# Kernel tuning notes

Measured on AMD Instinct MI355X. Metric: run time of the kernel, lower is better.

The kernel has to match this reference:

```python
import jax, jax.numpy as jnp
import numpy as np

# Module / shape constants (match init_kwargs and forward-path constants)
H = 8          # heads
DH = 80        # dim_head
QDIM = 640     # query_dim == inner_dim (context = x, self-attention content branch)
B = 1
NQ = 2048      # query tokens
NS = 2048      # injected style tokens
T = 1.2        # injection_config['T']  (attn_matrix_scale)
GAMMA = 0.3    # injection_config['gamma'] (q_mix)
LAMBDA_MAX = 2.5
TOPK = 128     # style_topk
STYLE_SCALE = 1.0
SCALE = DH ** -0.5


def _split_heads(t, h):
    # 'b n (h d) -> (b h) n d'
    b, n, hd = t.shape
    return t.reshape(b, n, h, hd // h).transpose(0, 2, 1, 3).reshape(b * h, n, hd // h)


def setup_inputs() -> dict:
    key = jax.random.key(0)
    ks = jax.random.split(key, 9)
    x = jax.random.normal(ks[0], (B, NQ, QDIM), jnp.float32)
    Q_c_injected = jax.random.normal(ks[1], (H, NQ, DH), jnp.float32) * 0.5
    K_s_injected = jax.random.normal(ks[2], (H, NS, DH), jnp.float32) * 0.5
    V_s_injected = jax.random.normal(ks[3], (H, NS, DH), jnp.float32) * 0.5
    # Learned params (nn.Linear weights are [out, in]; no bias on q/k/v)
    Wq = jax.random.normal(ks[4], (H * DH, QDIM), jnp.float32) * 0.02
    Wk = jax.random.normal(ks[5], (H * DH, QDIM), jnp.float32) * 0.02
    Wv = jax.random.normal(ks[6], (H * DH, QDIM), jnp.float32) * 0.02
    Wo = jax.random.normal(ks[7], (QDIM, H * DH), jnp.float32) * 0.02
    bo = jnp.zeros((QDIM,), jnp.float32)
    ada_gate = jnp.array([0.2], jnp.float32)
    return {"x": x, "Q_c_injected": Q_c_injected, "K_s_injected": K_s_injected,
            "V_s_injected": V_s_injected, "Wq": Wq, "Wk": Wk, "Wv": Wv,
            "Wo": Wo, "bo": bo, "ada_gate": ada_gate}


def reference(x, Q_c_injected, K_s_injected, V_s_injected, Wq, Wk, Wv, Wo, bo, ada_gate):
    b, n, _ = x.shape
    # Projections, context = x
    q_cs = _split_heads(x @ Wq.T, H)                    # (b h) n d
    k_cs = _split_heads(x @ Wk.T, H)                    # (b h) m d
    v_cs = _split_heads(x @ Wv.T, H)
    Q_c = jnp.tile(Q_c_injected, (b, 1, 1))             # torch.cat([Q_c]*b)
    q = Q_c * GAMMA + q_cs * (1.0 - GAMMA)              # Q_hat_cs
    K_s = jnp.tile(K_s_injected, (b, 1, 1))
    V_s = jnp.tile(V_s_injected, (b, 1, 1))

    style = jnp.einsum('bid,bjd->bij', q, K_s) * (T * SCALE)   # (bh) nq ns
    content = jnp.einsum('bid,bjd->bij', q, k_cs) * SCALE       # (bh) nq nc
    ns = style.shape[-1]
    s4 = style.reshape(b, H, n, ns)
    c4 = content.reshape(b, H, n, -1)

    # Per-head logsumexp gating between style and content branches
    r = jax.scipy.special.logsumexp(s4, axis=-1) - jax.scipy.special.logsumexp(c4, axis=-1)
    r = jnp.clip(r, -20.0, 20.0).mean(axis=1)           # (b, nq)
    lam = 1.0 + (LAMBDA_MAX - 1.0) * jax.nn.sigmoid(r)  # lambda_map
    style = (s4 * lam[:, None, :, None]).reshape(b * H, n, ns)

    # Top-k sparsification of style logits (scatter top-k values onto -inf canvas)
    vals, idx = jax.lax.top_k(style, TOPK)
    neg = jnp.finfo(style.dtype).min
    bi = jnp.arange(b * H)[:, None, None]
    ni = jnp.arange(n)[None, :, None]
    style = jnp.full_like(style, neg).at[bi, ni, idx].set(vals)

    logits = jnp.concatenate([style, content], axis=-1)
    attn = jax.nn.softmax(logits, axis=-1)
    v = jnp.concatenate([V_s * STYLE_SCALE, v_cs], axis=1)      # (bh) (ns+nc) d
    out = jnp.einsum('bij,bjd->bid', attn, v)

    # AdaIN-style modulation
    A = attn.reshape(b, H, n, -1)
    Vh = v.reshape(b, H, -1, DH)
    Qh = q.reshape(b, H, n, DH)
    Vmean = jnp.einsum('bhnm,bhmd->bhnd', A, Vh)
    mu = Qh.mean(axis=2, keepdims=True)
    var = Qh.var(axis=2, keepdims=True)                 # unbiased=False
    Qn = (Qh - mu) / jnp.sqrt(var + 1e-5)
    Vsq = jnp.einsum('bhnm,bhmd->bhnd', A, Vh * Vh)
    Vstd = jnp.sqrt(jnp.clip(Vsq - Vmean ** 2, 1e-5))
    out_mod = (Vstd * Qn + Vmean).reshape(b * H, n, DH)  # use_std_scale path

    g = jnp.tanh(ada_gate[0])                            # use_residual_gate
    out = out + g * (out_mod - out)
    out = out.reshape(b, H, n, DH).transpose(0, 2, 1, 3).reshape(b, n, H * DH)
    return out @ Wo.T + bo                               # to_out (dropout=0)
```

## Files before the change

kernel.cpp:

```cpp
#include <hip/hip_runtime.h>
#include <hip/hip_fp16.h>
#include <math.h>

#define NH 8
#define DH 80
#define NTOK 2048
#define QD 640
#define SCALE_F 0.11180339887498949f
#define TSCALE_F (1.2f * SCALE_F)
#define GAMMA_F 0.3f
#define LMAX_F 2.5f
#define TOPKN 128

typedef __attribute__((ext_vector_type(8))) short bf16x8;
typedef __attribute__((ext_vector_type(4))) float f32x4;
typedef __attribute__((ext_vector_type(4))) unsigned short u16x4;

#define OFF_QB   0u
#define OFF_OB   1310720u
#define OFF_QH   2621440u
#define OFF_QL   3407872u
#define OFF_KCH  4194304u
#define OFF_KSH  4980736u
#define OFF_KSL  5767168u
#define OFF_VCB  6553600u
#define OFF_VCQ  7208960u
#define OFF_VSB  7864320u
#define OFF_VSQ  8519680u
#define OFF_OP   9175040u
#define OFF_SP   14417920u
#define OFF_DEN  19660800u
#define OFF_MSZ  19726336u
#define OFF_LSZ  19791872u
#define OFF_MCZ  19857408u
#define OFF_LCZ  19922944u
#define OFF_M    19988480u
#define OFF_LAM  20004864u
#define OFF_THR  20006912u
#define OFF_MU   20023296u
#define OFF_RSTD 20023936u
#define OFF_S16  20024576u

static __device__ __forceinline__ unsigned short f2bf(float f) {
  unsigned u = __float_as_uint(f);
  return (unsigned short)((u + 0x7FFFu + ((u >> 16) & 1u)) >> 16);
}
static __device__ __forceinline__ float bf2f(unsigned short s) {
  return __uint_as_float(((unsigned)s) << 16);
}
static __device__ __forceinline__ unsigned sk16(unsigned u) {
  return (u & 0x8000u) ? (~u & 0xFFFFu) : (u | 0x8000u);
}

__global__ __launch_bounds__(256) void k_projmm(
    const float* __restrict__ x, const float* __restrict__ Wq,
    const float* __restrict__ Wk, const float* __restrict__ Wv,
    const float* __restrict__ Qc, float* __restrict__ qb,
    unsigned short* __restrict__ qh_, unsigned short* __restrict__ ql_,
    unsigned short* __restrict__ kch_,
    unsigned short* __restrict__ vcb_, unsigned short* __restrict__ vcq_)
{
  const float* W = (blockIdx.z == 0) ? Wq : ((blockIdx.z == 1) ? Wk : Wv);
  const int n0 = blockIdx.y * 64, c0 = blockIdx.x * 64;
  const int tid = threadIdx.x;
  const int w = tid >> 6, l = tid & 63;
  const int cc = l & 15, g = l >> 4;

  __shared__ unsigned short sXh[64 * 72];
  __shared__ unsigned short sXl[64 * 72];
  __shared__ unsigned short sWh[64 * 72];
  __shared__ unsigned short sWl[64 * 72];

  f32x4 D[4];
#pragma unroll
  for (int ct = 0; ct < 4; ++ct) D[ct] = (f32x4){0.f, 0.f, 0.f, 0.f};

  for (int k0 = 0; k0 < QD; k0 += 64) {
    __syncthreads();
#pragma unroll
    for (int it = 0; it < 4; ++it) {
      int f = tid + it * 256;
      int row = f >> 4, col4 = f & 15;
      float4 xa = *(const float4*)(x + (size_t)(n0 + row) * QD + k0 + col4 * 4);
      float4 wa = *(const float4*)(W + (size_t)(c0 + row) * QD + k0 + col4 * 4);
      u16x4 xh, xl, wh, wl;
      float xv[4] = {xa.x, xa.y, xa.z, xa.w};
      float wv[4] = {wa.x, wa.y, wa.z, wa.w};
#pragma unroll
      for (int j = 0; j < 4; ++j) {
        unsigned short h1 = f2bf(xv[j]);
        xh[j] = h1; xl[j] = f2bf(xv[j] - bf2f(h1));
        unsigned short h2 = f2bf(wv[j]);
        wh[j] = h2; wl[j] = f2bf(wv[j] - bf2f(h2));
      }
      *(u16x4*)&sXh[row * 72 + col4 * 4] = xh;
      *(u16x4*)&sXl[row * 72 + col4 * 4] = xl;
      *(u16x4*)&sWh[row * 72 + col4 * 4] = wh;
      *(u16x4*)&sWl[row * 72 + col4 * 4] = wl;
    }
    __syncthreads();
    bf16x8 ah[2], al[2];
#pragma unroll
    for (int kc = 0; kc < 2; ++kc) {
      ah[kc] = *(const bf16x8*)&sXh[(w * 16 + cc) * 72 + kc * 32 + g * 8];
      al[kc] = *(const bf16x8*)&sXl[(w * 16 + cc) * 72 + kc * 32 + g * 8];
    }
#pragma unroll
    for (int ct = 0; ct < 4; ++ct) {
#pragma unroll
      for (int kc = 0; kc < 2; ++kc) {
        bf16x8 bh = *(const bf16x8*)&sWh[(ct * 16 + cc) * 72 + kc * 32 + g * 8];
        bf16x8 bl = *(const bf16x8*)&sWl[(ct * 16 + cc) * 72 + kc * 32 + g * 8];
        D[ct] = __builtin_amdgcn_mfma_f32_16x16x32_bf16(ah[kc], bh, D[ct], 0, 0, 0);
        D[ct] = __builtin_amdgcn_mfma_f32_16x16x32_bf16(ah[kc], bl, D[ct], 0, 0, 0);
        D[ct] = __builtin_amdgcn_mfma_f32_16x16x32_bf16(al[kc], bh, D[ct], 0, 0, 0);
      }
    }
  }
#pragma unroll
  for (int ct = 0; ct < 4; ++ct) {
#pragma unroll
    for (int r = 0; r < 4; ++r) {
      int n = n0 + w * 16 + g * 4 + r;
      int ccol = c0 + ct * 16 + cc;
      int h = ccol / DH, d = ccol - h * DH;
      size_t i80 = ((size_t)h * NTOK + n) * 80 + d;
      size_t i96 = ((size_t)h * NTOK + n) * 96 + d;
      float val = D[ct][r];
      if (blockIdx.z == 0) {
        val = GAMMA_F * Qc[i80] + (1.f - GAMMA_F) * val;
        qb[i80] = val;
        unsigned short hs = f2bf(val);
        qh_[i96] = hs;
        ql_[i96] = f2bf(val - bf2f(hs));
      } else if (blockIdx.z == 1) {
        kch_[i96] = f2bf(val);
      } else {
        vcb_[i80] = f2bf(val);
        vcq_[i80] = f2bf(val * val);
      }
    }
  }
}

__global__ __launch_bounds__(384) void k_cvt(
    const float* __restrict__ Ks, const float* __restrict__ Vs,
    unsigned short* __restrict__ Ksh, unsigned short* __restrict__ Ksl,
    unsigned short* __restrict__ Vsb, unsigned short* __restrict__ Vsq,
    unsigned short* __restrict__ qh_, unsigned short* __restrict__ ql_,
    unsigned short* __restrict__ kch_)
{
  int h = blockIdx.y;
  int n = blockIdx.x * 4 + threadIdx.x / 96;
  int d = threadIdx.x % 96;
  size_t i80 = ((size_t)h * NTOK + n) * 80 + d;
  size_t i96 = ((size_t)h * NTOK + n) * 96 + d;
  if (d < 80) {
    float v = Ks[i80];
    unsigned short hs = f2bf(v);
    Ksh[i96] = hs; Ksl[i96] = f2bf(v - bf2f(hs));
    float vv = Vs[i80];
    Vsb[i80] = f2bf(vv); Vsq[i80] = f2bf(vv * vv);
  } else {
    Ksh[i96] = 0; Ksl[i96] = 0; qh_[i96] = 0; ql_[i96] = 0; kch_[i96] = 0;
  }
}

__global__ __launch_bounds__(128) void k_qstats(
    const float* __restrict__ qb, float* __restrict__ mu, float* __restrict__ rstd)
{
  const int h = blockIdx.x / DH, d = blockIdx.x % DH;
  const int tid = threadIdx.x;
  float s = 0.f, s2 = 0.f;
  for (int n = tid; n < NTOK; n += 128) {
    float v = qb[((size_t)h * NTOK + n) * 80 + d];
    s += v; s2 = fmaf(v, v, s2);
  }
#pragma unroll
  for (int off = 32; off; off >>= 1) { s += __shfl_xor(s, off, 64); s2 += __shfl_xor(s2, off, 64); }
  __shared__ float sh[4];
  if ((tid & 63) == 0) { sh[(tid >> 6) * 2] = s; sh[(tid >> 6) * 2 + 1] = s2; }
  __syncthreads();
  if (tid == 0) {
    float S = sh[0] + sh[2], S2 = sh[1] + sh[3];
    float mval = S * (1.f / NTOK);
    float var = S2 * (1.f / NTOK) - mval * mval;
    mu[h * DH + d] = mval;
    rstd[h * DH + d] = rsqrtf(var + 1e-5f);
  }
}

__global__ __launch_bounds__(256) void k_passA(
    const unsigned short* __restrict__ qh_, const unsigned short* __restrict__ ql_,
    const unsigned short* __restrict__ Ksh, const unsigned short* __restrict__ Ksl,
    const unsigned short* __restrict__ kch_,
    unsigned short* __restrict__ S16, float* __restrict__ mSz, float* __restrict__ lSz,
    float* __restrict__ mCz, float* __restrict__ lCz)
{
  const int bid = blockIdx.x;
  const int swz = (bid & 7) * 128 + (bid >> 3);
  const int q0 = (swz & 31) * 64;
  const int h  = (swz >> 5) & 7;
  const int z  = swz >> 8;
  const int tid = threadIdx.x;
  const int w = tid >> 6, l = tid & 63;
  const int c = l & 15, g = l >> 4;

  __shared__ unsigned short sKh[64 * 104];
  __shared__ unsigned short sKl[64 * 104];

  bf16x8 qhf[3], qlf[3];
  {
    const size_t qrow = ((size_t)h * NTOK + q0 + w * 16 + c) * 96;
#pragma unroll
    for (int kc = 0; kc < 3; ++kc) {
      qhf[kc] = *(const bf16x8*)(qh_ + qrow + kc * 32 + g * 8);
      qlf[kc] = *(const bf16x8*)(ql_ + qrow + kc * 32 + g * 8);
    }
  }
  float m[4], lse[4], mc[4], lc[4];
#pragma unroll
  for (int r = 0; r < 4; ++r) { m[r] = -INFINITY; lse[r] = 0.f; mc[r] = -INFINITY; lc[r] = 0.f; }

  for (int t = 0; t < 8; ++t) {
    const size_t kbase = ((size_t)h * NTOK + z * 512 + t * 64) * 96;
    __syncthreads();
    for (int f = tid; f < 768; f += 256) {
      int row = f / 12, ch = f % 12;
      *(bf16x8*)(sKh + row * 104 + ch * 8) = *(const bf16x8*)(Ksh + kbase + row * 96 + ch * 8);
      *(bf16x8*)(sKl + row * 104 + ch * 8) = *(const bf16x8*)(Ksl + kbase + row * 96 + ch * 8);
    }
    __syncthreads();
#pragma unroll
    for (int ct = 0; ct < 4; ++ct) {
      f32x4 D = {0.f, 0.f, 0.f, 0.f};
      const int krow = (ct * 16 + c) * 104 + g * 8;
#pragma unroll
      for (int kc = 0; kc < 3; ++kc) {
        bf16x8 bh = *(const bf16x8*)(sKh + krow + kc * 32);
        D = __builtin_amdgcn_mfma_f32_16x16x32_bf16(qhf[kc], bh, D, 0, 0, 0);
      }
#pragma unroll
      for (int kc = 0; kc < 3; ++kc) {
        bf16x8 bl = *(const bf16x8*)(sKl + krow + kc * 32);
        D = __builtin_amdgcn_mfma_f32_16x16x32_bf16(qhf[kc], bl, D, 0, 0, 0);
      }
#pragma unroll
      for (int kc = 0; kc < 3; ++kc) {
        bf16x8 bh = *(const bf16x8*)(sKh + krow + kc * 32);
        D = __builtin_amdgcn_mfma_f32_16x16x32_bf16(qlf[kc], bh, D, 0, 0, 0);
      }
#pragma unroll
      for (int r = 0; r < 4; ++r) {
        float s = D[r] * TSCALE_F;
        __half hh = __float2half(s);
        S16[((size_t)h * NTOK + q0 + w * 16 + g * 4 + r) * 2048 + z * 512 + t * 64 + ct * 16 + c] =
            __half_as_ushort(hh);
        float mn = fmaxf(m[r], s);
        lse[r] = lse[r] * __expf(m[r] - mn) + __expf(s - mn);
        m[r] = mn;
      }
    }
  }
  for (int t = 0; t < 8; ++t) {
    const size_t kbase = ((size_t)h * NTOK + z * 512 + t * 64) * 96;
    __syncthreads();
    for (int f = tid; f < 768; f += 256) {
      int row = f / 12, ch = f % 12;
      *(bf16x8*)(sKh + row * 104 + ch * 8) = *(const bf16x8*)(kch_ + kbase + row * 96 + ch * 8);
    }
    __syncthreads();
#pragma unroll
    for (int ct = 0; ct < 4; ++ct) {
      f32x4 D = {0.f, 0.f, 0.f, 0.f};
      const int krow = (ct * 16 + c) * 104 + g * 8;
#pragma unroll
      for (int kc = 0; kc < 3; ++kc) {
        bf16x8 bh = *(const bf16x8*)(sKh + krow + kc * 32);
        D = __builtin_amdgcn_mfma_f32_16x16x32_bf16(qhf[kc], bh, D, 0, 0, 0);
      }
#pragma unroll
      for (int r = 0; r < 4; ++r) {
        float s = D[r] * SCALE_F;
        float mn = fmaxf(mc[r], s);
        lc[r] = lc[r] * __expf(mc[r] - mn) + __expf(s - mn);
        mc[r] = mn;
      }
    }
  }
#pragma unroll
  for (int off = 1; off < 16; off <<= 1) {
#pragma unroll
    for (int r = 0; r < 4; ++r) {
      float mo = __shfl_xor(m[r], off, 64), lo = __shfl_xor(lse[r], off, 64);
      float mn = fmaxf(m[r], mo);
      lse[r] = lse[r] * __expf(m[r] - mn) + lo * __expf(mo - mn);
      m[r] = mn;
      float mo2 = __shfl_xor(mc[r], off, 64), lo2 = __shfl_xor(lc[r], off, 64);
      float mn2 = fmaxf(mc[r], mo2);
      lc[r] = lc[r] * __expf(mc[r] - mn2) + lo2 * __expf(mo2 - mn2);
      mc[r] = mn2;
    }
  }
  if (c == 0) {
    size_t base = (size_t)(z * 8 + h) * NTOK + q0 + w * 16 + g * 4;
#pragma unroll
    for (int r = 0; r < 4; ++r) {
      mSz[base + r] = m[r]; lSz[base + r] = lse[r];
      mCz[base + r] = mc[r]; lCz[base + r] = lc[r];
    }
  }
}

__global__ __launch_bounds__(256) void k_gate(
    const float* __restrict__ mSz, const float* __restrict__ lSz,
    const float* __restrict__ mCz, const float* __restrict__ lCz,
    float* __restrict__ M_, float* __restrict__ lam_)
{
  int n = blockIdx.x * 256 + threadIdx.x;
  if (n >= NTOK) return;
  float msf[NH], mcf[NH], sum = 0.f;
#pragma unroll
  for (int h = 0; h < NH; ++h) {
    float mm = -INFINITY, cm = -INFINITY;
#pragma unroll
    for (int zz = 0; zz < 4; ++zz) {
      mm = fmaxf(mm, mSz[(size_t)(zz * 8 + h) * NTOK + n]);
      cm = fmaxf(cm, mCz[(size_t)(zz * 8 + h) * NTOK + n]);
    }
    float ls = 0.f, lcs = 0.f;
#pragma unroll
    for (int zz = 0; zz < 4; ++zz) {
      ls  += lSz[(size_t)(zz * 8 + h) * NTOK + n] * __expf(mSz[(size_t)(zz * 8 + h) * NTOK + n] - mm);
      lcs += lCz[(size_t)(zz * 8 + h) * NTOK + n] * __expf(mCz[(size_t)(zz * 8 + h) * NTOK + n] - cm);
    }
    float lse_s = mm + __logf(ls);
    float lse_c = cm + __logf(lcs);
    msf[h] = mm; mcf[h] = cm;
    sum += fminf(fmaxf(lse_s - lse_c, -20.f), 20.f);
  }
  float lam = 1.f + (LMAX_F - 1.f) * (1.f / (1.f + __expf(-sum * (1.f / NH))));
  lam_[n] = lam;
#pragma unroll
  for (int h = 0; h < NH; ++h)
    M_[h * NTOK + n] = fmaxf(lam * msf[h], mcf[h]);
}

__global__ __launch_bounds__(512) void k_topk(const unsigned short* __restrict__ S16,
                                              unsigned* __restrict__ thr_)
{
  const int h = blockIdx.y;
  const int n = blockIdx.x * 8 + (threadIdx.x >> 6);
  const int l = threadIdx.x & 63;
  const unsigned short* Srow = S16 + ((size_t)h * NTOK + n) * 2048;
  unsigned kv[32];
#pragma unroll
  for (int t = 0; t < 4; ++t) {
    uint4 v = ((const uint4*)Srow)[t * 64 + l];
    unsigned dw[4] = {v.x, v.y, v.z, v.w};
#pragma unroll
    for (int i = 0; i < 8; ++i) {
      unsigned u = (dw[i >> 1] >> ((i & 1) * 16)) & 0xFFFFu;
      kv[t * 8 + i] = sk16(u);
    }
  }
  unsigned klo = 0u, khi = 65536u;
  for (int it = 0; it < 16; ++it) {
    unsigned mid = (klo + khi) >> 1;
    int cnt = 0;
#pragma unroll
    for (int t = 0; t < 32; ++t)
      cnt += __popcll(__ballot(kv[t] >= mid));
    if (cnt == TOPKN) { klo = mid; break; }
    if (cnt > TOPKN) klo = mid; else khi = mid;
    if (khi - klo <= 1u) break;
  }
  if (l == 0) thr_[h * NTOK + n] = klo;
}

__global__ __launch_bounds__(256) void k_passB(
    const unsigned short* __restrict__ qh_, const unsigned short* __restrict__ kch_,
    const unsigned short* __restrict__ Vsb, const unsigned short* __restrict__ Vsq,
    const unsigned short* __restrict__ vcb, const unsigned short* __restrict__ vcq,
    const unsigned short* __restrict__ S16,
    const float* __restrict__ M_, const float* __restrict__ lam_,
    const unsigned* __restrict__ thr_,
    float* __restrict__ oP, float* __restrict__ sP, float* __restrict__ denP)
{
  const int bid = blockIdx.x;
  const int swz = (bid & 7) * 128 + (bid >> 3);
  const int q0 = (swz & 31) * 64;
  const int h  = (swz >> 5) & 7;
  const int z  = swz >> 8;
  const int tid = threadIdx.x;
  const int w = tid >> 6, l = tid & 63;
  const int c = l & 15, g = l >> 4;

  __shared__ char arena[45568];
  unsigned short* S_lds   = (unsigned short*)arena;
  unsigned short* kch_lds = (unsigned short*)arena;
  unsigned short* P_lds   = (unsigned short*)(arena + 13312);
  unsigned short* vT      = (unsigned short*)(arena + 22528);
  unsigned short* vqT     = (unsigned short*)(arena + 34048);
  __shared__ float Mr[64], lamr[64], den_l[64];
  __shared__ unsigned thrr[64];

  if (tid < 64) {
    int n = q0 + tid;
    Mr[tid] = M_[h * NTOK + n];
    lamr[tid] = lam_[n];
    thrr[tid] = thr_[h * NTOK + n];
    den_l[tid] = 0.f;
  }
  bf16x8 qhf[3];
  {
    const size_t qrow = ((size_t)h * NTOK + q0 + w * 16 + c) * 96;
#pragma unroll
    for (int kc = 0; kc < 3; ++kc)
      qhf[kc] = *(const bf16x8*)(qh_ + qrow + kc * 32 + g * 8);
  }
  __syncthreads();
  const float myLam = lamr[w * 16 + c], myM = Mr[w * 16 + c];
  const unsigned myThr = thrr[w * 16 + c];
  float myM4[4];
#pragma unroll
  for (int r = 0; r < 4; ++r) myM4[r] = Mr[w * 16 + g * 4 + r];

  f32x4 oacc[5], sacc[5];
#pragma unroll
  for (int dt = 0; dt < 5; ++dt) { oacc[dt] = (f32x4){0.f,0.f,0.f,0.f}; sacc[dt] = (f32x4){0.f,0.f,0.f,0.f}; }
  float denS = 0.f, denC[4] = {0.f, 0.f, 0.f, 0.f};

  for (int t = 0; t < 8; ++t) {
    const int k0 = z * 512 + t * 64;
    __syncthreads();
    for (int f = tid; f < 512; f += 256) {
      int row = f >> 3, ch = f & 7;
      *(uint4*)&S_lds[row * 72 + ch * 8] =
          *(const uint4*)(S16 + ((size_t)h * NTOK + q0 + row) * 2048 + k0 + ch * 8);
    }
    for (int f = tid; f < 320; f += 256) {
      int kp = f & 31, ch = f >> 5;
      const size_t vb = ((size_t)h * NTOK + k0 + kp * 2) * 80 + ch * 8;
      bf16x8 a = *(const bf16x8*)(Vsb + vb);
      bf16x8 b = *(const bf16x8*)(Vsb + vb + 80);
      bf16x8 aq = *(const bf16x8*)(Vsq + vb);
      bf16x8 bq = *(const bf16x8*)(Vsq + vb + 80);
#pragma unroll
      for (int j = 0; j < 8; ++j) {
        int d = ch * 8 + j;
        *(unsigned*)&vT[d * 72 + kp * 2]  = ((unsigned)(unsigned short)b[j] << 16) | (unsigned short)a[j];
        *(unsigned*)&vqT[d * 72 + kp * 2] = ((unsigned)(unsigned short)bq[j] << 16) | (unsigned short)aq[j];
      }
    }
    __syncthreads();
    bf16x8 pa[2];
#pragma unroll
    for (int kc = 0; kc < 2; ++kc) {
      uint4 sv = *(const uint4*)&S_lds[(w * 16 + c) * 72 + kc * 32 + g * 8];
      unsigned dw[4] = {sv.x, sv.y, sv.z, sv.w};
      bf16x8 pk;
#pragma unroll
      for (int i = 0; i < 8; ++i) {
        unsigned u = (dw[i >> 1] >> ((i & 1) * 16)) & 0xFFFFu;
        float s = __half2float(__ushort_as_half((unsigned short)u));
        float wv = (sk16(u) >= myThr) ? __expf(myLam * s - myM) : 0.f;
        denS += wv;
        pk[i] = (short)f2bf(wv);
      }
      pa[kc] = pk;
    }
#pragma unroll
    for (int dt = 0; dt < 5; ++dt) {
#pragma unroll
      for (int kc = 0; kc < 2; ++kc) {
        bf16x8 bv  = *(const bf16x8*)&vT[(dt * 16 + c) * 72 + kc * 32 + g * 8];
        bf16x8 bvq = *(const bf16x8*)&vqT[(dt * 16 + c) * 72 + kc * 32 + g * 8];
        oacc[dt] = __builtin_amdgcn_mfma_f32_16x16x32_bf16(pa[kc], bv, oacc[dt], 0, 0, 0);
        sacc[dt] = __builtin_amdgcn_mfma_f32_16x16x32_bf16(pa[kc], bvq, sacc[dt], 0, 0, 0);
      }
    }
  }
  for (int t = 0; t < 8; ++t) {
    const int k0 = z * 512 + t * 64;
    __syncthreads();
    for (int f = tid; f < 768; f += 256) {
      int row = f / 12, ch = f % 12;
      *(bf16x8*)(kch_lds + row * 104 + ch * 8) =
          *(const bf16x8*)(kch_ + ((size_t)h * NTOK + k0 + row) * 96 + ch * 8);
    }
    for (int f = tid; f < 320; f += 256) {
      int kp = f & 31, ch = f >> 5;
      const size_t vb = ((size_t)h * NTOK + k0 + kp * 2) * 80 + ch * 8;
      bf16x8 a = *(const bf16x8*)(vcb + vb);
      bf16x8 b = *(const bf16x8*)(vcb + vb + 80);
      bf16x8 aq = *(const bf16x8*)(vcq + vb);
      bf16x8 bq = *(const bf16x8*)(vcq + vb + 80);
#pragma unroll
      for (int j = 0; j < 8; ++j) {
        int d = ch * 8 + j;
        *(unsigned*)&vT[d * 72 + kp * 2]  = ((unsigned)(unsigned short)b[j] << 16) | (unsigned short)a[j];
        *(unsigned*)&vqT[d * 72 + kp * 2] = ((unsigned)(unsigned short)bq[j] << 16) | (unsigned short)aq[j];
      }
    }
    __syncthreads();
#pragma unroll
    for (int ct = 0; ct < 4; ++ct) {
      f32x4 D = {0.f, 0.f, 0.f, 0.f};
      const int krow = (ct * 16 + c) * 104 + g * 8;
#pragma unroll
      for (int kc = 0; kc < 3; ++kc) {
        bf16x8 bh = *(const bf16x8*)(kch_lds + krow + kc * 32);
        D = __builtin_amdgcn_mfma_f32_16x16x32_bf16(qhf[kc], bh, D, 0, 0, 0);
      }
#pragma unroll
      for (int r = 0; r < 4; ++r) {
        float s = D[r] * SCALE_F;
        float wv = __expf(s - myM4[r]);
        denC[r] += wv;
        P_lds[w * 1152 + (g * 4 + r) * 72 + ct * 16 + c] = f2bf(wv);
      }
    }
    __syncthreads();
    bf16x8 pa0 = *(const bf16x8*)(P_lds + w * 1152 + c * 72 + g * 8);
    bf16x8 pa1 = *(const bf16x8*)(P_lds + w * 1152 + c * 72 + 32 + g * 8);
#pragma unroll
    for (int dt = 0; dt < 5; ++dt) {
      bf16x8 bv0  = *(const bf16x8*)&vT[(dt * 16 + c) * 72 + g * 8];
      bf16x8 bvq0 = *(const bf16x8*)&vqT[(dt * 16 + c) * 72 + g * 8];
      bf16x8 bv1  = *(const bf16x8*)&vT[(dt * 16 + c) * 72 + 32 + g * 8];
      bf16x8 bvq1 = *(const bf16x8*)&vqT[(dt * 16 + c) * 72 + 32 + g * 8];
      oacc[dt] = __builtin_amdgcn_mfma_f32_16x16x32_bf16(pa0, bv0, oacc[dt], 0, 0, 0);
      sacc[dt] = __builtin_amdgcn_mfma_f32_16x16x32_bf16(pa0, bvq0, sacc[dt], 0, 0, 0);
      oacc[dt] = __builtin_amdgcn_mfma_f32_16x16x32_bf16(pa1, bv1, oacc[dt], 0, 0, 0);
      sacc[dt] = __builtin_amdgcn_mfma_f32_16x16x32_bf16(pa1, bvq1, sacc[dt], 0, 0, 0);
    }
  }
  denS += __shfl_xor(denS, 16, 64);
  denS += __shfl_xor(denS, 32, 64);
#pragma unroll
  for (int off = 1; off < 16; off <<= 1)
#pragma unroll
    for (int r = 0; r < 4; ++r) denC[r] += __shfl_xor(denC[r], off, 64);
  if (l < 16) atomicAdd(&den_l[w * 16 + l], denS);
  if (c == 0) {
#pragma unroll
    for (int r = 0; r < 4; ++r) atomicAdd(&den_l[w * 16 + g * 4 + r], denC[r]);
  }
  __syncthreads();
  const size_t base = (size_t)(z * 8 + h) * NTOK + q0 + w * 16;
#pragma unroll
  for (int dt = 0; dt < 5; ++dt)
#pragma unroll
    for (int r = 0; r < 4; ++r) {
      size_t o = (base + g * 4 + r) * 80 + dt * 16 + c;
      oP[o] = oacc[dt][r];
      sP[o] = sacc[dt][r];
    }
  if (tid < 64) denP[(size_t)(z * 8 + h) * NTOK + q0 + tid] = den_l[tid];
}

__global__ __launch_bounds__(256) void k_fin(
    const float* __restrict__ oP, const float* __restrict__ sP,
    const float* __restrict__ denP, const float* __restrict__ qb,
    const float* __restrict__ mu, const float* __restrict__ rstd,
    const float* __restrict__ gate, float* __restrict__ Ob)
{
  int idx = blockIdx.x * 256 + threadIdx.x;
  int h = idx / (NTOK * 80);
  int rem = idx - h * (NTOK * 80);
  int n = rem / 80, d = rem - n * 80;
  float den = 0.f, o = 0.f, sq = 0.f;
#pragma unroll
  for (int zz = 0; zz < 4; ++zz) {
    den += denP[(size_t)(zz * 8 + h) * NTOK + n];
    size_t p = ((size_t)(zz * 8 + h) * NTOK + n) * 80 + d;
    o += oP[p];
    sq += sP[p];
  }
  o /= den;
  sq /= den;
  float vstd = sqrtf(fmaxf(sq - o * o, 1e-5f));
  float g = tanhf(gate[0]);
  float qn = (qb[((size_t)h * NTOK + n) * 80 + d] - mu[h * DH + d]) * rstd[h * DH + d];
  Ob[(size_t)n * QD + h * DH + d] = fmaf(g * vstd, qn, o);
}

__global__ __launch_bounds__(256) void k_finalmm(
    const float* __restrict__ A, const float* __restrict__ W,
    const float* __restrict__ bias, float* __restrict__ out)
{
  const int n0 = blockIdx.y * 64, c0 = blockIdx.x * 64;
  const int tid = threadIdx.x;
  const int w = tid >> 6, l = tid & 63;
  const int cc = l & 15, g = l >> 4;

  __shared__ unsigned short sXh[64 * 72];
  __shared__ unsigned short sXl[64 * 72];
  __shared__ unsigned short sWh[64 * 72];
  __shared__ unsigned short sWl[64 * 72];

  f32x4 D[4];
#pragma unroll
  for (int ct = 0; ct < 4; ++ct) D[ct] = (f32x4){0.f, 0.f, 0.f, 0.f};

  for (int k0 = 0; k0 < QD; k0 += 64) {
    __syncthreads();
#pragma unroll
    for (int it = 0; it < 4; ++it) {
      int f = tid + it * 256;
      int row = f >> 4, col4 = f & 15;
      float4 xa = *(const float4*)(A + (size_t)(n0 + row) * QD + k0 + col4 * 4);
      float4 wa = *(const float4*)(W + (size_t)(c0 + row) * QD + k0 + col4 * 4);
      u16x4 xh, xl, wh, wl;
      float xv[4] = {xa.x, xa.y, xa.z, xa.w};
      float wv[4] = {wa.x, wa.y, wa.z, wa.w};
#pragma unroll
      for (int j = 0; j < 4; ++j) {
        unsigned short h1 = f2bf(xv[j]);
        xh[j] = h1; xl[j] = f2bf(xv[j] - bf2f(h1));
        unsigned short h2 = f2bf(wv[j]);
        wh[j] = h2; wl[j] = f2bf(wv[j] - bf2f(h2));
      }
      *(u16x4*)&sXh[row * 72 + col4 * 4] = xh;
      *(u16x4*)&sXl[row * 72 + col4 * 4] = xl;
      *(u16x4*)&sWh[row * 72 + col4 * 4] = wh;
      *(u16x4*)&sWl[row * 72 + col4 * 4] = wl;
    }
    __syncthreads();
    bf16x8 ah[2], al[2];
#pragma unroll
    for (int kc = 0; kc < 2; ++kc) {
      ah[kc] = *(const bf16x8*)&sXh[(w * 16 + cc) * 72 + kc * 32 + g * 8];
      al[kc] = *(const bf16x8*)&sXl[(w * 16 + cc) * 72 + kc * 32 + g * 8];
    }
#pragma unroll
    for (int ct = 0; ct < 4; ++ct) {
#pragma unroll
      for (int kc = 0; kc < 2; ++kc) {
        bf16x8 bh = *(const bf16x8*)&sWh[(ct * 16 + cc) * 72 + kc * 32 + g * 8];
        bf16x8 bl = *(const bf16x8*)&sWl[(ct * 16 + cc) * 72 + kc * 32 + g * 8];
        D[ct] = __builtin_amdgcn_mfma_f32_16x16x32_bf16(ah[kc], bh, D[ct], 0, 0, 0);
        D[ct] = __builtin_amdgcn_mfma_f32_16x16x32_bf16(ah[kc], bl, D[ct], 0, 0, 0);
        D[ct] = __builtin_amdgcn_mfma_f32_16x16x32_bf16(al[kc], bh, D[ct], 0, 0, 0);
      }
    }
  }
#pragma unroll
  for (int ct = 0; ct < 4; ++ct) {
#pragma unroll
    for (int r = 0; r < 4; ++r) {
      int n = n0 + w * 16 + g * 4 + r;
      int ccol = c0 + ct * 16 + cc;
      out[(size_t)n * QD + ccol] = D[ct][r] + bias[ccol];
    }
  }
}

extern "C" void kernel_launch(void* const* d_in, const int* in_sizes, int n_in,
                              void* d_out, int out_size, void* d_ws, size_t ws_size,
                              hipStream_t stream) {
  const float* x    = (const float*)d_in[0];
  const float* Qc   = (const float*)d_in[1];
  const float* Ks   = (const float*)d_in[2];
  const float* Vs   = (const float*)d_in[3];
  const float* Wq   = (const float*)d_in[4];
  const float* Wk   = (const float*)d_in[5];
  const float* Wv   = (const float*)d_in[6];
  const float* Wo   = (const float*)d_in[7];
  const float* bo   = (const float*)d_in[8];
  const float* gate = (const float*)d_in[9];
  float* out = (float*)d_out;
  float* w = (float*)d_ws;

  float* qb   = w + OFF_QB;
  float* Ob   = w + OFF_OB;
  unsigned short* qh_  = (unsigned short*)(w + OFF_QH);
  unsigned short* ql_  = (unsigned short*)(w + OFF_QL);
  unsigned short* kch_ = (unsigned short*)(w + OFF_KCH);
  unsigned short* Ksh  = (unsigned short*)(w + OFF_KSH);
  unsigned short* Ksl  = (unsigned short*)(w + OFF_KSL);
  unsigned short* vcb  = (unsigned short*)(w + OFF_VCB);
  unsigned short* vcq  = (unsigned short*)(w + OFF_VCQ);
  unsigned short* Vsb  = (unsigned short*)(w + OFF_VSB);
  unsigned short* Vsq  = (unsigned short*)(w + OFF_VSQ);
  float* oP   = w + OFF_OP;
  float* sP   = w + OFF_SP;
  float* denP = w + OFF_DEN;
  float* mSz  = w + OFF_MSZ;
  float* lSz  = w + OFF_LSZ;
  float* mCz  = w + OFF_MCZ;
  float* lCz  = w + OFF_LCZ;
  float* M_   = w + OFF_M;
  float* lam_ = w + OFF_LAM;
  unsigned* thr_ = (unsigned*)(w + OFF_THR);
  float* mu   = w + OFF_MU;
  float* rstd = w + OFF_RSTD;
  unsigned short* S16 = (unsigned short*)(w + OFF_S16);

  k_projmm<<<dim3(10, 32, 3), 256, 0, stream>>>(x, Wq, Wk, Wv, Qc, qb, qh_, ql_, kch_, vcb, vcq);
  k_cvt<<<dim3(512, 8), 384, 0, stream>>>(Ks, Vs, Ksh, Ksl, Vsb, Vsq, qh_, ql_, kch_);
  k_qstats<<<dim3(640), 128, 0, stream>>>(qb, mu, rstd);
  k_passA<<<dim3(1024), 256, 0, stream>>>(qh_, ql_, Ksh, Ksl, kch_, S16, mSz, lSz, mCz, lCz);
  k_gate<<<dim3(8), 256, 0, stream>>>(mSz, lSz, mCz, lCz, M_, lam_);
  k_topk<<<dim3(256, 8), 512, 0, stream>>>(S16, thr_);
  k_passB<<<dim3(1024), 256, 0, stream>>>(qh_, kch_, Vsb, Vsq, vcb, vcq, S16, M_, lam_, thr_, oP, sP, denP);
  k_fin<<<dim3(5120), 256, 0, stream>>>(oP, sP, denP, qb, mu, rstd, gate, Ob);
  k_finalmm<<<dim3(10, 32), 256, 0, stream>>>(Ob, Wo, bo, out);
}
```

Before: 293.6 us.

## Store V and V² pre-transposed in global memory to simplify passB staging

The producers (k_projmm for content V, k_cvt for style V) now write bf16 V and V² in a transposed [h][d][token] layout, and k_cvt stages the transpose through LDS. passB then loads contiguous 8-element vectors straight into its transposed LDS tiles, dropping the per-element repacking loop. One __syncthreads between the P_lds writes and reads in the content loop is also removed. That barrier removal could be a race if P_lds rows are read by other waves, though the indexing appears per-wave. The transposed writes in k_projmm are strided scalar stores, which may cost more there.

```diff
diff --git a/kernel.cpp b/kernel.cpp
--- a/kernel.cpp
+++ b/kernel.cpp
@@ -23,10 +23,10 @@
 #define OFF_KCH  4194304u
 #define OFF_KSH  4980736u
 #define OFF_KSL  5767168u
-#define OFF_VCB  6553600u
-#define OFF_VCQ  7208960u
-#define OFF_VSB  7864320u
-#define OFF_VSQ  8519680u
+#define OFF_VCT  6553600u
+#define OFF_VCQT 7208960u
+#define OFF_VST  7864320u
+#define OFF_VSQT 8519680u
 #define OFF_OP   9175040u
 #define OFF_SP   14417920u
 #define OFF_DEN  19660800u
@@ -58,7 +58,7 @@
     const float* __restrict__ Qc, float* __restrict__ qb,
     unsigned short* __restrict__ qh_, unsigned short* __restrict__ ql_,
     unsigned short* __restrict__ kch_,
-    unsigned short* __restrict__ vcb_, unsigned short* __restrict__ vcq_)
+    unsigned short* __restrict__ vct_, unsigned short* __restrict__ vcqt_)
 {
   const float* W = (blockIdx.z == 0) ? Wq : ((blockIdx.z == 1) ? Wk : Wv);
   const int n0 = blockIdx.y * 64, c0 = blockIdx.x * 64;
@@ -136,33 +136,61 @@
       } else if (blockIdx.z == 1) {
         kch_[i96] = f2bf(val);
       } else {
-        vcb_[i80] = f2bf(val);
-        vcq_[i80] = f2bf(val * val);
-      }
-    }
-  }
-}
-
-__global__ __launch_bounds__(384) void k_cvt(
+        size_t iT = (((size_t)h * 80 + d) << 11) + n;
+        vct_[iT]  = f2bf(val);
+        vcqt_[iT] = f2bf(val * val);
+      }
+    }
+  }
+}
+
+__global__ __launch_bounds__(256) void k_cvt(
     const float* __restrict__ Ks, const float* __restrict__ Vs,
     unsigned short* __restrict__ Ksh, unsigned short* __restrict__ Ksl,
-    unsigned short* __restrict__ Vsb, unsigned short* __restrict__ Vsq,
+    unsigned short* __restrict__ VTs, unsigned short* __restrict__ VTqs,
     unsigned short* __restrict__ qh_, unsigned short* __restrict__ ql_,
     unsigned short* __restrict__ kch_)
 {
-  int h = blockIdx.y;
-  int n = blockIdx.x * 4 + threadIdx.x / 96;
-  int d = threadIdx.x % 96;
-  size_t i80 = ((size_t)h * NTOK + n) * 80 + d;
-  size_t i96 = ((size_t)h * NTOK + n) * 96 + d;
-  if (d < 80) {
-    float v = Ks[i80];
-    unsigned short hs = f2bf(v);
-    Ksh[i96] = hs; Ksl[i96] = f2bf(v - bf2f(hs));
-    float vv = Vs[i80];
-    Vsb[i80] = f2bf(vv); Vsq[i80] = f2bf(vv * vv);
-  } else {
+  const int h = blockIdx.y;
+  const int n0 = blockIdx.x * 64;
+  const int tid = threadIdx.x;
+  __shared__ unsigned short sVT[80 * 68];
+  __shared__ unsigned short sVQ[80 * 68];
+
+  for (int f = tid; f < 1280; f += 256) {
+    int rr = f / 20, dc = f % 20;
+    size_t i80 = ((size_t)h * NTOK + n0 + rr) * 80 + dc * 4;
+    size_t i96 = ((size_t)h * NTOK + n0 + rr) * 96 + dc * 4;
+    float4 kv = *(const float4*)(Ks + i80);
+    float kvv[4] = {kv.x, kv.y, kv.z, kv.w};
+    u16x4 kh, kl;
+#pragma unroll
+    for (int j = 0; j < 4; ++j) {
+      unsigned short hs = f2bf(kvv[j]);
+      kh[j] = hs; kl[j] = f2bf(kvv[j] - bf2f(hs));
+    }
+    *(u16x4*)(Ksh + i96) = kh;
+    *(u16x4*)(Ksl + i96) = kl;
+    float4 vv = *(const float4*)(Vs + i80);
+    float vvv[4] = {vv.x, vv.y, vv.z, vv.w};
+#pragma unroll
+    for (int j = 0; j < 4; ++j) {
+      int d = dc * 4 + j;
+      sVT[d * 68 + rr] = f2bf(vvv[j]);
+      sVQ[d * 68 + rr] = f2bf(vvv[j] * vvv[j]);
+    }
+  }
+  for (int f = tid; f < 1024; f += 256) {
+    int rr = f >> 4, dcol = 80 + (f & 15);
+    size_t i96 = ((size_t)h * NTOK + n0 + rr) * 96 + dcol;
     Ksh[i96] = 0; Ksl[i96] = 0; qh_[i96] = 0; ql_[i96] = 0; kch_[i96] = 0;
+  }
+  __syncthreads();
+  for (int f = tid; f < 640; f += 256) {
+    int d = f >> 3, kp8 = f & 7;
+    size_t iT = (((size_t)h * 80 + d) << 11) + n0 + kp8 * 8;
+    *(bf16x8*)(VTs + iT)  = *(const bf16x8*)&sVT[d * 68 + kp8 * 8];
+    *(bf16x8*)(VTqs + iT) = *(const bf16x8*)&sVQ[d * 68 + kp8 * 8];
   }
 }
 
@@ -380,8 +408,8 @@
 
 __global__ __launch_bounds__(256) void k_passB(
     const unsigned short* __restrict__ qh_, const unsigned short* __restrict__ kch_,
-    const unsigned short* __restrict__ Vsb, const unsigned short* __restrict__ Vsq,
-    const unsigned short* __restrict__ vcb, const unsigned short* __restrict__ vcq,
+    const unsigned short* __restrict__ VTs, const unsigned short* __restrict__ VTqs,
+    const unsigned short* __restrict__ VTc, const unsigned short* __restrict__ VTqc,
     const unsigned short* __restrict__ S16,
     const float* __restrict__ M_, const float* __restrict__ lam_,
     const unsigned* __restrict__ thr_,
@@ -439,19 +467,11 @@
       *(uint4*)&S_lds[row * 72 + ch * 8] =
           *(const uint4*)(S16 + ((size_t)h * NTOK + q0 + row) * 2048 + k0 + ch * 8);
     }
-    for (int f = tid; f < 320; f += 256) {
-      int kp = f & 31, ch = f >> 5;
-      const size_t vb = ((size_t)h * NTOK + k0 + kp * 2) * 80 + ch * 8;
-      bf16x8 a = *(const bf16x8*)(Vsb + vb);
-      bf16x8 b = *(const bf16x8*)(Vsb + vb + 80);
-      bf16x8 aq = *(const bf16x8*)(Vsq + vb);
-      bf16x8 bq = *(const bf16x8*)(Vsq + vb + 80);
-#pragma unroll
-      for (int j = 0; j < 8; ++j) {
-        int d = ch * 8 + j;
-        *(unsigned*)&vT[d * 72 + kp * 2]  = ((unsigned)(unsigned short)b[j] << 16) | (unsigned short)a[j];
-        *(unsigned*)&vqT[d * 72 + kp * 2] = ((unsigned)(unsigned short)bq[j] << 16) | (unsigned short)aq[j];
-      }
+    for (int f = tid; f < 640; f += 256) {
+      int d = f >> 3, kp8 = f & 7;
+      size_t iT = (((size_t)h * 80 + d) << 11) + k0 + kp8 * 8;
+      *(bf16x8*)&vT[d * 72 + kp8 * 8]  = *(const bf16x8*)(VTs + iT);
+      *(bf16x8*)&vqT[d * 72 + kp8 * 8] = *(const bf16x8*)(VTqs + iT);
     }
     __syncthreads();
     bf16x8 pa[2];
@@ -489,19 +509,11 @@
       *(bf16x8*)(kch_lds + row * 104 + ch * 8) =
           *(const bf16x8*)(kch_ + ((size_t)h * NTOK + k0 + row) * 96 + ch * 8);
     }
-    for (int f = tid; f < 320; f += 256) {
-      int kp = f & 31, ch = f >> 5;
-      const size_t vb = ((size_t)h * NTOK + k0 + kp * 2) * 80 + ch * 8;
-      bf16x8 a = *(const bf16x8*)(vcb + vb);
-      bf16x8 b = *(const bf16x8*)(vcb + vb + 80);
-      bf16x8 aq = *(const bf16x8*)(vcq + vb);
-      bf16x8 bq = *(const bf16x8*)(vcq + vb + 80);
-#pragma unroll
-      for (int j = 0; j < 8; ++j) {
-        int d = ch * 8 + j;
-        *(unsigned*)&vT[d * 72 + kp * 2]  = ((unsigned)(unsigned short)b[j] << 16) | (unsigned short)a[j];
-        *(unsigned*)&vqT[d * 72 + kp * 2] = ((unsigned)(unsigned short)bq[j] << 16) | (unsigned short)aq[j];
-      }
+    for (int f = tid; f < 640; f += 256) {
+      int d = f >> 3, kp8 = f & 7;
+      size_t iT = (((size_t)h * 80 + d) << 11) + k0 + kp8 * 8;
+      *(bf16x8*)&vT[d * 72 + kp8 * 8]  = *(const bf16x8*)(VTc + iT);
+      *(bf16x8*)&vqT[d * 72 + kp8 * 8] = *(const bf16x8*)(VTqc + iT);
     }
     __syncthreads();
 #pragma unroll
@@ -521,7 +533,6 @@
         P_lds[w * 1152 + (g * 4 + r) * 72 + ct * 16 + c] = f2bf(wv);
       }
     }
-    __syncthreads();
     bf16x8 pa0 = *(const bf16x8*)(P_lds + w * 1152 + c * 72 + g * 8);
     bf16x8 pa1 = *(const bf16x8*)(P_lds + w * 1152 + c * 72 + 32 + g * 8);
 #pragma unroll
@@ -680,10 +691,10 @@
   unsigned short* kch_ = (unsigned short*)(w + OFF_KCH);
   unsigned short* Ksh  = (unsigned short*)(w + OFF_KSH);
   unsigned short* Ksl  = (unsigned short*)(w + OFF_KSL);
-  unsigned short* vcb  = (unsigned short*)(w + OFF_VCB);
-  unsigned short* vcq  = (unsigned short*)(w + OFF_VCQ);
-  unsigned short* Vsb  = (unsigned short*)(w + OFF_VSB);
-  unsigned short* Vsq  = (unsigned short*)(w + OFF_VSQ);
+  unsigned short* VTc  = (unsigned short*)(w + OFF_VCT);
+  unsigned short* VTqc = (unsigned short*)(w + OFF_VCQT);
+  unsigned short* VTs  = (unsigned short*)(w + OFF_VST);
+  unsigned short* VTqs = (unsigned short*)(w + OFF_VSQT);
   float* oP   = w + OFF_OP;
   float* sP   = w + OFF_SP;
   float* denP = w + OFF_DEN;
@@ -698,13 +709,13 @@
   float* rstd = w + OFF_RSTD;
   unsigned short* S16 = (unsigned short*)(w + OFF_S16);
 
-  k_projmm<<<dim3(10, 32, 3), 256, 0, stream>>>(x, Wq, Wk, Wv, Qc, qb, qh_, ql_, kch_, vcb, vcq);
-  k_cvt<<<dim3(512, 8), 384, 0, stream>>>(Ks, Vs, Ksh, Ksl, Vsb, Vsq, qh_, ql_, kch_);
+  k_projmm<<<dim3(10, 32, 3), 256, 0, stream>>>(x, Wq, Wk, Wv, Qc, qb, qh_, ql_, kch_, VTc, VTqc);
+  k_cvt<<<dim3(32, 8), 256, 0, stream>>>(Ks, Vs, Ksh, Ksl, VTs, VTqs, qh_, ql_, kch_);
   k_qstats<<<dim3(640), 128, 0, stream>>>(qb, mu, rstd);
   k_passA<<<dim3(1024), 256, 0, stream>>>(qh_, ql_, Ksh, Ksl, kch_, S16, mSz, lSz, mCz, lCz);
   k_gate<<<dim3(8), 256, 0, stream>>>(mSz, lSz, mCz, lCz, M_, lam_);
   k_topk<<<dim3(256, 8), 512, 0, stream>>>(S16, thr_);
-  k_passB<<<dim3(1024), 256, 0, stream>>>(qh_, kch_, Vsb, Vsq, vcb, vcq, S16, M_, lam_, thr_, oP, sP, denP);
+  k_passB<<<dim3(1024), 256, 0, stream>>>(qh_, kch_, VTs, VTqs, VTc, VTqc, S16, M_, lam_, thr_, oP, sP, denP);
   k_fin<<<dim3(5120), 256, 0, stream>>>(oP, sP, denP, qb, mu, rstd, gate, Ob);
   k_finalmm<<<dim3(10, 32), 256, 0, stream>>>(Ob, Wo, bo, out);
 }
```

After: 304.2 us. 1.04x slower.
